# Kernel optimization log

Hardware: AMD Instinct MI355X
Metric: run time of the kernel (lower is better)

## Reference

```python
import jax, jax.numpy as jnp
import numpy as np

B, S, D, H = 2, 2048, 768, 12
DK = D // H


def setup_inputs() -> dict:
    key = jax.random.key(0)
    ks = jax.random.split(key, 12)
    s = 1.0 / np.sqrt(D)
    inp = {
        "query": jax.random.normal(ks[0], (B, S, D), jnp.float32),
        "key_": jax.random.normal(ks[1], (B, S, D), jnp.float32),
        "value": jax.random.normal(ks[2], (B, S, D), jnp.float32),
        # causal mask: 1 where attention allowed, 0 where blocked
        "mask": jnp.tril(jnp.ones((S, S), jnp.int32))[None, None, :, :],
        "W_q": jax.random.normal(ks[3], (D, D), jnp.float32) * s,
        "b_q": jnp.zeros((D,), jnp.float32),
        "W_k": jax.random.normal(ks[4], (D, D), jnp.float32) * s,
        "b_k": jnp.zeros((D,), jnp.float32),
        "W_v": jax.random.normal(ks[5], (D, D), jnp.float32) * s,
        "b_v": jnp.zeros((D,), jnp.float32),
        "W_o": jax.random.normal(ks[6], (D, D), jnp.float32) * s,
        "b_o": jnp.zeros((D,), jnp.float32),
    }
    return inp


def reference(query, key_, value, mask, W_q, b_q, W_k, b_k, W_v, b_v, W_o, b_o):
    # Linear projections (torch Linear: x @ W.T + b; here W stored as [in,out])
    Q = query @ W_q + b_q
    K = key_ @ W_k + b_k
    V = value @ W_v + b_v
    # [B,S,D] -> [B,H,S,dk]
    Q = Q.reshape(B, S, H, DK).transpose(0, 2, 1, 3)
    K = K.reshape(B, S, H, DK).transpose(0, 2, 1, 3)
    V = V.reshape(B, S, H, DK).transpose(0, 2, 1, 3)
    # NOTE: original module does NOT scale by 1/sqrt(d_k) -- faithful.
    scores = jnp.einsum('bhqd,bhkd->bhqk', Q, K)  # [B,H,S,S]
    scores = jnp.where(mask == 0, -jnp.inf, scores)
    attn = jax.nn.softmax(scores, axis=-1)
    out = jnp.einsum('bhqk,bhkd->bhqd', attn, V)  # [B,H,S,dk]
    out = out.transpose(0, 2, 1, 3).reshape(B, S, D)
    return out @ W_o + b_o
```

## Files before the change

### kernel.cpp

```cpp
#include <hip/hip_runtime.h>
#include <hip/hip_bf16.h>
#include <math.h>
#include <stdint.h>

constexpr int BATCH  = 2;
constexpr int SEQ    = 2048;
constexpr int DMODEL = 768;
constexpr int NH     = 12;
constexpr int HD     = 64;
constexpr int NTOK   = BATCH * SEQ;
constexpr float LOG2E = 1.4426950408889634f;

typedef __attribute__((ext_vector_type(8))) short     short8;
typedef __attribute__((ext_vector_type(8))) _Float16  half8;
typedef __attribute__((ext_vector_type(4))) float     floatx4;

#define DEVINL __device__ __forceinline__

DEVINL floatx4 mfma16(short8 a, short8 b, floatx4 c) {
    return __builtin_amdgcn_mfma_f32_16x16x32_bf16(a, b, c, 0, 0, 0);
}
DEVINL floatx4 mfma16h(half8 a, half8 b, floatx4 c) {
    return __builtin_amdgcn_mfma_f32_16x16x32_f16(a, b, c, 0, 0, 0);
}
DEVINL __hip_bfloat16 f2b(float x) { return __float2bfloat16(x); }

DEVINL void load16_lds(const void* g, void* l) {
    __builtin_amdgcn_global_load_lds(
        reinterpret_cast<const __attribute__((address_space(1))) unsigned int*>(
            reinterpret_cast<uintptr_t>(g)),
        reinterpret_cast<__attribute__((address_space(3))) unsigned int*>(
            reinterpret_cast<uintptr_t>(l)),
        16, 0, 0);
}

__global__ void pack_wt4(const float* __restrict__ W0, const float* __restrict__ W1,
                         const float* __restrict__ W2, const float* __restrict__ W3,
                         _Float16* H0, _Float16* H1, _Float16* H2, _Float16* H3) {
    int z = blockIdx.z;
    const float* W = (z == 0) ? W0 : (z == 1) ? W1 : (z == 2) ? W2 : W3;
    _Float16* H = (z == 0) ? H0 : (z == 1) ? H1 : (z == 2) ? H2 : H3;
    float sc = (z == 0) ? LOG2E : 1.0f;
    __shared__ float t[32][33];
    int k0 = blockIdx.x * 32, n0 = blockIdx.y * 32;
    int tx = threadIdx.x, ty = threadIdx.y;
    for (int i = ty; i < 32; i += 8)
        t[i][tx] = W[(size_t)(k0 + i) * DMODEL + n0 + tx];
    __syncthreads();
    for (int i = ty; i < 32; i += 8)
        H[(size_t)(n0 + i) * DMODEL + k0 + tx] = (_Float16)(t[tx][i] * sc);
}

__global__ void conv_h(const float* __restrict__ q, const float* __restrict__ k,
                       const float* __restrict__ v,
                       _Float16* qf, _Float16* kf, _Float16* vf) {
    int y = blockIdx.y;
    const float* src = (y == 0) ? q : (y == 1) ? k : v;
    _Float16* dst = (y == 0) ? qf : (y == 1) ? kf : vf;
    size_t base = ((size_t)blockIdx.x * 256 + threadIdx.x) * 8;
    float4 a = *(const float4*)(src + base);
    float4 b = *(const float4*)(src + base + 4);
    half8 o;
    o[0] = (_Float16)a.x; o[1] = (_Float16)a.y; o[2] = (_Float16)a.z; o[3] = (_Float16)a.w;
    o[4] = (_Float16)b.x; o[5] = (_Float16)b.y; o[6] = (_Float16)b.z; o[7] = (_Float16)b.w;
    *(half8*)(dst + base) = o;
}

DEVINL void stage_ab(const uint16_t* A, const uint16_t* B,
                     char* buf, int m0, int n0, int k0, int tid, int wv) {
#pragma unroll
    for (int i = 0; i < 4; ++i) {
        int e = i * 256 + tid;
        int row = e >> 3, c8 = (e & 7) ^ (row & 7);
        load16_lds(A + (size_t)(m0 + row) * DMODEL + k0 + c8 * 8,
                   buf + i * 4096 + wv * 1024);
    }
#pragma unroll
    for (int i = 0; i < 2; ++i) {
        int e = i * 256 + tid;
        int row = e >> 3, c8 = (e & 7) ^ (row & 7);
        load16_lds(B + (size_t)(n0 + row) * DMODEL + k0 + c8 * 8,
                   buf + 16384 + i * 4096 + wv * 1024);
    }
}

__global__ __launch_bounds__(256) void gemm_qkv(
    const uint16_t* __restrict__ qf, const uint16_t* __restrict__ kf,
    const uint16_t* __restrict__ vf,
    const uint16_t* __restrict__ Wq, const uint16_t* __restrict__ Wk,
    const uint16_t* __restrict__ Wv,
    const float* __restrict__ bq, const float* __restrict__ bk,
    const float* __restrict__ bv,
    _Float16* Qf, _Float16* Kf, __hip_bfloat16* Vt) {
    __shared__ __align__(16) char smem[49152];

    int z = blockIdx.z;
    const uint16_t* A = (z == 0) ? qf : (z == 1) ? kf : vf;
    const uint16_t* B = (z == 0) ? Wq : (z == 1) ? Wk : Wv;
    const float* bias = (z == 0) ? bq : (z == 1) ? bk : bv;
    float bscale = (z == 0) ? LOG2E : 1.0f;

    int tid = threadIdx.x;
    int wv = tid >> 6, lane = tid & 63, quad = lane >> 4, ln = lane & 15;
    int mw = wv & 1, nw = wv >> 1;
    int m0 = blockIdx.x * 128, n0 = blockIdx.y * 64;
    int sw = (ln & 7) * 16;

    floatx4 acc[4][2];
#pragma unroll
    for (int f = 0; f < 4; ++f)
#pragma unroll
        for (int g = 0; g < 2; ++g) acc[f][g] = floatx4{0.f, 0.f, 0.f, 0.f};

    stage_ab(A, B, smem, m0, n0, 0, tid, wv);

    for (int s = 0; s < 12; ++s) {
        __syncthreads();
        if (s + 1 < 12)
            stage_ab(A, B, smem + ((s + 1) & 1) * 24576, m0, n0, (s + 1) * 64, tid, wv);
        char* buf = smem + (s & 1) * 24576;
#pragma unroll
        for (int ks = 0; ks < 2; ++ks) {
            half8 ah[4], bh2[2];
#pragma unroll
            for (int f = 0; f < 4; ++f) {
                int row = mw * 64 + f * 16 + ln;
                ah[f] = *(const half8*)(buf + row * 128 + ((ks * 64 + quad * 16) ^ sw));
            }
#pragma unroll
            for (int g = 0; g < 2; ++g) {
                int row = nw * 32 + g * 16 + ln;
                bh2[g] = *(const half8*)(buf + 16384 + row * 128 + ((ks * 64 + quad * 16) ^ sw));
            }
#pragma unroll
            for (int f = 0; f < 4; ++f)
#pragma unroll
                for (int g = 0; g < 2; ++g)
                    acc[f][g] = mfma16h(ah[f], bh2[g], acc[f][g]);
        }
    }

    if (z == 2) {
        __syncthreads();
        __hip_bfloat16* T = (__hip_bfloat16*)smem;
#pragma unroll
        for (int f = 0; f < 4; ++f)
#pragma unroll
            for (int g = 0; g < 2; ++g) {
                int nl = nw * 32 + g * 16 + ln;
                float bvv = bias[n0 + nl];
#pragma unroll
                for (int rr = 0; rr < 4; ++rr) {
                    int ml = mw * 64 + f * 16 + quad * 4 + rr;
                    T[nl * 136 + ml] = f2b(acc[f][g][rr] + bvv);
                }
            }
        __syncthreads();
        int h = n0 >> 6, b = m0 >> 11;
        __hip_bfloat16* dst = Vt + (size_t)(b * NH + h) * HD * SEQ;
#pragma unroll
        for (int i = 0; i < 4; ++i) {
            int cid = i * 256 + tid;
            int d = cid >> 4, ch = cid & 15;
            short8 v = *(const short8*)(T + d * 136 + ch * 8);
            *(short8*)(dst + (size_t)d * SEQ + (m0 & (SEQ - 1)) + ch * 8) = v;
        }
    } else {
        _Float16* o0 = (z == 0) ? Qf : Kf;
#pragma unroll
        for (int f = 0; f < 4; ++f)
#pragma unroll
            for (int g = 0; g < 2; ++g) {
                int ncol = n0 + nw * 32 + g * 16 + ln;
                float bvv = bias[ncol] * bscale;
#pragma unroll
                for (int rr = 0; rr < 4; ++rr) {
                    int mrow = m0 + mw * 64 + f * 16 + quad * 4 + rr;
                    int b = mrow >> 11, s = mrow & (SEQ - 1);
                    int h = ncol >> 6, d = ncol & (HD - 1);
                    o0[((size_t)(b * NH + h) * SEQ + s) * HD + d] =
                        (_Float16)(acc[f][g][rr] + bvv);
                }
            }
    }
}

__global__ __launch_bounds__(256) void flash_k(
    const _Float16* __restrict__ Qf, const _Float16* __restrict__ Kf,
    const __hip_bfloat16* __restrict__ Vt,
    float* __restrict__ Oacc, float* __restrict__ Lacc) {
    int slot = blockIdx.x, bh = blockIdx.y;
    int qti, kv0, kv1;
    if (slot < 16) {
        qti = 15 - (slot >> 1);
        int hf = slot & 1;
        kv0 = hf * (qti + 1);
        kv1 = kv0 + qti + 1;
    } else {
        qti = 23 - slot;
        kv0 = 0;
        kv1 = 2 * qti + 2;
    }

    int tid = threadIdx.x;
    int wv = tid >> 6, lane = tid & 63, quad = lane >> 4, ln = lane & 15;
    int sw = (ln & 7) * 16;

    const _Float16* Qb = Qf + (size_t)bh * SEQ * HD;
    const uint16_t* Kb = (const uint16_t*)Kf + (size_t)bh * SEQ * HD;
    const uint16_t* Vb = (const uint16_t*)Vt + (size_t)bh * HD * SEQ;

    int qr0 = qti * 128 + wv * 32;

    __shared__ __align__(16) char smem[32768 + 4 * 16 * 72 * 2];
    __hip_bfloat16* sP = (__hip_bfloat16*)(smem + 32768) + wv * 16 * 72;

    auto stage = [&](int kv, int bsel) {
        char* buf = smem + bsel * 16384;
        int kb = kv * 64;
#pragma unroll
        for (int i = 0; i < 2; ++i) {
            int e = i * 256 + tid;
            int row = e >> 3, c8 = (e & 7) ^ (row & 7);
            int ldso = i * 4096 + wv * 1024;
            load16_lds(Kb + (size_t)(kb + row) * HD + c8 * 8, buf + ldso);
            load16_lds(Vb + (size_t)row * SEQ + kb + c8 * 8, buf + 8192 + ldso);
        }
    };

    stage(kv0, 0);

    half8 aQ[2][2];
#pragma unroll
    for (int rg = 0; rg < 2; ++rg)
#pragma unroll
        for (int ks = 0; ks < 2; ++ks)
            aQ[rg][ks] = *(const half8*)(Qb + (size_t)(qr0 + rg * 16 + ln) * HD +
                                         ks * 32 + quad * 8);

    short8 vone;
#pragma unroll
    for (int i = 0; i < 8; ++i) vone[i] = (short)0x3F80;

    floatx4 accO[2][4], accL[2];
#pragma unroll
    for (int rg = 0; rg < 2; ++rg) {
        accL[rg] = floatx4{0.f, 0.f, 0.f, 0.f};
#pragma unroll
        for (int j = 0; j < 4; ++j) accO[rg][j] = floatx4{0.f, 0.f, 0.f, 0.f};
    }

    for (int kv = kv0; kv < kv1; ++kv) {
        int ib = (kv - kv0) & 1;
        __syncthreads();
        if (kv + 1 < kv1) stage(kv + 1, ib ^ 1);
        const char* sK = smem + ib * 16384;
        const char* sV = sK + 8192;
        int kb = kv * 64;

        floatx4 accS[2][4];
#pragma unroll
        for (int rg = 0; rg < 2; ++rg)
#pragma unroll
            for (int cc = 0; cc < 4; ++cc) accS[rg][cc] = floatx4{0.f, 0.f, 0.f, 0.f};
#pragma unroll
        for (int cc = 0; cc < 4; ++cc)
#pragma unroll
            for (int ks = 0; ks < 2; ++ks) {
                int off = (cc * 16 + ln) * 128 + ((ks * 64 + quad * 16) ^ sw);
                half8 bK = *(const half8*)(sK + off);
                accS[0][cc] = mfma16h(aQ[0][ks], bK, accS[0][cc]);
                accS[1][cc] = mfma16h(aQ[1][ks], bK, accS[1][cc]);
            }

        short8 aP[2][2];
#pragma unroll
        for (int rg = 0; rg < 2; ++rg) {
            bool domask = (kb + 63 > qr0 + rg * 16);
#pragma unroll
            for (int rr = 0; rr < 4; ++rr) {
                int qg = qr0 + rg * 16 + quad * 4 + rr;
#pragma unroll
                for (int cc = 0; cc < 4; ++cc) {
                    float s = accS[rg][cc][rr];
                    if (domask && (kb + cc * 16 + ln > qg)) s = -INFINITY;
                    sP[(quad * 4 + rr) * 72 + cc * 16 + ln] =
                        f2b(__builtin_amdgcn_exp2f(s));
                }
            }
#pragma unroll
            for (int ks = 0; ks < 2; ++ks)
                aP[rg][ks] = *(const short8*)(sP + ln * 72 + ks * 32 + quad * 8);
            accL[rg] = mfma16(aP[rg][0], vone, accL[rg]);
            accL[rg] = mfma16(aP[rg][1], vone, accL[rg]);
        }

#pragma unroll
        for (int cc = 0; cc < 4; ++cc)
#pragma unroll
            for (int ks = 0; ks < 2; ++ks) {
                int off = (cc * 16 + ln) * 128 + ((ks * 64 + quad * 16) ^ sw);
                short8 bV = *(const short8*)(sV + off);
                accO[0][cc] = mfma16(aP[0][ks], bV, accO[0][cc]);
                accO[1][cc] = mfma16(aP[1][ks], bV, accO[1][cc]);
            }
    }

    float* Ob = Oacc + (size_t)bh * SEQ * HD;
#pragma unroll
    for (int rg = 0; rg < 2; ++rg)
#pragma unroll
        for (int cc = 0; cc < 4; ++cc)
#pragma unroll
            for (int rr = 0; rr < 4; ++rr) {
                int s = qr0 + rg * 16 + quad * 4 + rr;
                unsafeAtomicAdd(&Ob[(size_t)s * HD + cc * 16 + ln], accO[rg][cc][rr]);
            }
    if (ln == 0) {
#pragma unroll
        for (int rg = 0; rg < 2; ++rg)
#pragma unroll
            for (int rr = 0; rr < 4; ++rr)
                unsafeAtomicAdd(&Lacc[bh * SEQ + qr0 + rg * 16 + quad * 4 + rr],
                                accL[rg][rr]);
    }
}

__global__ void combine_k(const float* __restrict__ Oacc, const float* __restrict__ Lacc,
                          _Float16* __restrict__ attn) {
    int idx = blockIdx.x * 256 + threadIdx.x;
    int d8 = idx & 7;
    int rest = idx >> 3;
    int s = rest & (SEQ - 1);
    int bh = rest >> 11;
    int b = bh / NH, h = bh % NH;
    float inv = 1.0f / Lacc[bh * SEQ + s];
    const float* src = Oacc + ((size_t)bh * SEQ + s) * HD + d8 * 8;
    float4 a = *(const float4*)src;
    float4 c = *(const float4*)(src + 4);
    half8 o;
    o[0] = (_Float16)(a.x * inv); o[1] = (_Float16)(a.y * inv);
    o[2] = (_Float16)(a.z * inv); o[3] = (_Float16)(a.w * inv);
    o[4] = (_Float16)(c.x * inv); o[5] = (_Float16)(c.y * inv);
    o[6] = (_Float16)(c.z * inv); o[7] = (_Float16)(c.w * inv);
    *(half8*)(attn + ((size_t)(b * SEQ + s)) * DMODEL + h * HD + d8 * 8) = o;
}

__global__ __launch_bounds__(256) void gemm_o(
    const uint16_t* __restrict__ A, const uint16_t* __restrict__ B,
    const float* __restrict__ bias, float* __restrict__ out) {
    __shared__ __align__(16) char smem[49152];

    int tid = threadIdx.x;
    int wv = tid >> 6, lane = tid & 63, quad = lane >> 4, ln = lane & 15;
    int mw = wv & 1, nw = wv >> 1;
    int m0 = blockIdx.x * 128, n0 = blockIdx.y * 64;
    int sw = (ln & 7) * 16;

    floatx4 acc[4][2];
#pragma unroll
    for (int f = 0; f < 4; ++f)
#pragma unroll
        for (int g = 0; g < 2; ++g) acc[f][g] = floatx4{0.f, 0.f, 0.f, 0.f};

    stage_ab(A, B, smem, m0, n0, 0, tid, wv);

    for (int s = 0; s < 12; ++s) {
        __syncthreads();
        if (s + 1 < 12)
            stage_ab(A, B, smem + ((s + 1) & 1) * 24576, m0, n0, (s + 1) * 64, tid, wv);
        char* buf = smem + (s & 1) * 24576;
#pragma unroll
        for (int ks = 0; ks < 2; ++ks) {
            half8 ah[4], bh2[2];
#pragma unroll
            for (int f = 0; f < 4; ++f) {
                int row = mw * 64 + f * 16 + ln;
                ah[f] = *(const half8*)(buf + row * 128 + ((ks * 64 + quad * 16) ^ sw));
            }
#pragma unroll
            for (int g = 0; g < 2; ++g) {
                int row = nw * 32 + g * 16 + ln;
                bh2[g] = *(const half8*)(buf + 16384 + row * 128 + ((ks * 64 + quad * 16) ^ sw));
            }
#pragma unroll
            for (int f = 0; f < 4; ++f)
#pragma unroll
                for (int g = 0; g < 2; ++g)
                    acc[f][g] = mfma16h(ah[f], bh2[g], acc[f][g]);
        }
    }
#pragma unroll
    for (int f = 0; f < 4; ++f)
#pragma unroll
        for (int g = 0; g < 2; ++g) {
            int ncol = n0 + nw * 32 + g * 16 + ln;
            float bvv = bias[ncol];
#pragma unroll
            for (int rr = 0; rr < 4; ++rr) {
                int mrow = m0 + mw * 64 + f * 16 + quad * 4 + rr;
                out[(size_t)mrow * DMODEL + ncol] = acc[f][g][rr] + bvv;
            }
        }
}

extern "C" void kernel_launch(void* const* d_in, const int* in_sizes, int n_in,
                              void* d_out, int out_size, void* d_ws, size_t ws_size,
                              hipStream_t stream) {
    const float* query = (const float*)d_in[0];
    const float* key_  = (const float*)d_in[1];
    const float* value = (const float*)d_in[2];
    const float* W_q = (const float*)d_in[4];
    const float* b_q = (const float*)d_in[5];
    const float* W_k = (const float*)d_in[6];
    const float* b_k = (const float*)d_in[7];
    const float* W_v = (const float*)d_in[8];
    const float* b_v = (const float*)d_in[9];
    const float* W_o = (const float*)d_in[10];
    const float* b_o = (const float*)d_in[11];

    constexpr size_t WSZ = (size_t)DMODEL * DMODEL;
    constexpr size_t QSZ = (size_t)BATCH * NH * SEQ * HD;
    constexpr size_t OSZ = QSZ;
    constexpr size_t LSZ = (size_t)BATCH * NH * SEQ;

    char* w = (char*)d_ws;
    _Float16* Wq = (_Float16*)w; w += WSZ * 2;
    _Float16* Wk = (_Float16*)w; w += WSZ * 2;
    _Float16* Wv = (_Float16*)w; w += WSZ * 2;
    _Float16* Wo = (_Float16*)w; w += WSZ * 2;
    _Float16* qf = (_Float16*)w; w += QSZ * 2;
    _Float16* kf = (_Float16*)w; w += QSZ * 2;
    _Float16* vf = (_Float16*)w; w += QSZ * 2;
    _Float16* Qf_ = (_Float16*)w; w += QSZ * 2;
    _Float16* Kf_ = (_Float16*)w; w += QSZ * 2;
    __hip_bfloat16* Vt_ = (__hip_bfloat16*)w; w += QSZ * 2;
    _Float16* attn_ = (_Float16*)w; w += QSZ * 2;
    float* Oacc = (float*)qf;
    float* Lacc = Oacc + OSZ;

    pack_wt4<<<dim3(24, 24, 4), dim3(32, 8), 0, stream>>>(
        W_q, W_k, W_v, W_o, Wq, Wk, Wv, Wo);
    conv_h<<<dim3(NTOK * DMODEL / 2048, 3), 256, 0, stream>>>(
        query, key_, value, qf, kf, vf);

    gemm_qkv<<<dim3(NTOK / 128, DMODEL / 64, 3), 256, 0, stream>>>(
        (const uint16_t*)qf, (const uint16_t*)kf, (const uint16_t*)vf,
        (const uint16_t*)Wq, (const uint16_t*)Wk, (const uint16_t*)Wv,
        b_q, b_k, b_v, Qf_, Kf_, Vt_);

    (void)hipMemsetAsync(Oacc, 0, (OSZ + LSZ) * sizeof(float), stream);

    flash_k<<<dim3(24, BATCH * NH), 256, 0, stream>>>(Qf_, Kf_, Vt_, Oacc, Lacc);

    combine_k<<<dim3(BATCH * NH * SEQ * 8 / 256), 256, 0, stream>>>(Oacc, Lacc, attn_);

    gemm_o<<<dim3(NTOK / 128, DMODEL / 64), 256, 0, stream>>>(
        (const uint16_t*)attn_, (const uint16_t*)Wo, b_o, (float*)d_out);
}
```

Measured before the change: 198.7 us.

## Merge prep kernels and stage GEMM epilogues through LDS for coalesced stores

Folds the weight transpose/pack and the input fp16 conversion into a single launch using a z-dimension split with a grid-stride loop. It also rewrites the Q/K projection epilogue and the output-projection epilogue to write results into swizzled shared memory first, then issue 16-byte coalesced global stores instead of scattered 2- or 4-byte per-lane stores. This removes one kernel launch and uncoalesced write traffic, at the cost of extra barriers and LDS round trips.

```diff
diff --git a/kernel.cpp b/kernel.cpp
--- a/kernel.cpp
+++ b/kernel.cpp
@@ -34,36 +34,43 @@
         16, 0, 0);
 }
 
-__global__ void pack_wt4(const float* __restrict__ W0, const float* __restrict__ W1,
-                         const float* __restrict__ W2, const float* __restrict__ W3,
-                         _Float16* H0, _Float16* H1, _Float16* H2, _Float16* H3) {
-    int z = blockIdx.z;
-    const float* W = (z == 0) ? W0 : (z == 1) ? W1 : (z == 2) ? W2 : W3;
-    _Float16* H = (z == 0) ? H0 : (z == 1) ? H1 : (z == 2) ? H2 : H3;
-    float sc = (z == 0) ? LOG2E : 1.0f;
-    __shared__ float t[32][33];
-    int k0 = blockIdx.x * 32, n0 = blockIdx.y * 32;
-    int tx = threadIdx.x, ty = threadIdx.y;
-    for (int i = ty; i < 32; i += 8)
-        t[i][tx] = W[(size_t)(k0 + i) * DMODEL + n0 + tx];
-    __syncthreads();
-    for (int i = ty; i < 32; i += 8)
-        H[(size_t)(n0 + i) * DMODEL + k0 + tx] = (_Float16)(t[tx][i] * sc);
-}
-
-__global__ void conv_h(const float* __restrict__ q, const float* __restrict__ k,
+__global__ void prep_k(const float* __restrict__ W0, const float* __restrict__ W1,
+                       const float* __restrict__ W2, const float* __restrict__ W3,
+                       _Float16* H0, _Float16* H1, _Float16* H2, _Float16* H3,
+                       const float* __restrict__ q, const float* __restrict__ k,
                        const float* __restrict__ v,
                        _Float16* qf, _Float16* kf, _Float16* vf) {
-    int y = blockIdx.y;
-    const float* src = (y == 0) ? q : (y == 1) ? k : v;
-    _Float16* dst = (y == 0) ? qf : (y == 1) ? kf : vf;
-    size_t base = ((size_t)blockIdx.x * 256 + threadIdx.x) * 8;
-    float4 a = *(const float4*)(src + base);
-    float4 b = *(const float4*)(src + base + 4);
-    half8 o;
-    o[0] = (_Float16)a.x; o[1] = (_Float16)a.y; o[2] = (_Float16)a.z; o[3] = (_Float16)a.w;
-    o[4] = (_Float16)b.x; o[5] = (_Float16)b.y; o[6] = (_Float16)b.z; o[7] = (_Float16)b.w;
-    *(half8*)(dst + base) = o;
+    int z = blockIdx.z;
+    int tid = threadIdx.x;
+    if (z < 4) {
+        const float* W = (z == 0) ? W0 : (z == 1) ? W1 : (z == 2) ? W2 : W3;
+        _Float16* H = (z == 0) ? H0 : (z == 1) ? H1 : (z == 2) ? H2 : H3;
+        float sc = (z == 0) ? LOG2E : 1.0f;
+        __shared__ float t[32][33];
+        int k0 = blockIdx.x * 32, n0 = blockIdx.y * 32;
+        int tx = tid & 31, ty = tid >> 5;
+        for (int i = ty; i < 32; i += 8)
+            t[i][tx] = W[(size_t)(k0 + i) * DMODEL + n0 + tx];
+        __syncthreads();
+        for (int i = ty; i < 32; i += 8)
+            H[(size_t)(n0 + i) * DMODEL + k0 + tx] = (_Float16)(t[tx][i] * sc);
+    } else {
+        const float* src = (z == 4) ? q : (z == 5) ? k : v;
+        _Float16* dst = (z == 4) ? qf : (z == 5) ? kf : vf;
+        constexpr int NCH = NTOK * DMODEL / 8;
+        int flat = (blockIdx.y * 24 + blockIdx.x) * 256 + tid;
+        for (int c = flat; c < NCH; c += 24 * 24 * 256) {
+            size_t base = (size_t)c * 8;
+            float4 a = *(const float4*)(src + base);
+            float4 b = *(const float4*)(src + base + 4);
+            half8 o;
+            o[0] = (_Float16)a.x; o[1] = (_Float16)a.y;
+            o[2] = (_Float16)a.z; o[3] = (_Float16)a.w;
+            o[4] = (_Float16)b.x; o[5] = (_Float16)b.y;
+            o[6] = (_Float16)b.z; o[7] = (_Float16)b.w;
+            *(half8*)(dst + base) = o;
+        }
+    }
 }
 
 DEVINL void stage_ab(const uint16_t* A, const uint16_t* B,
@@ -139,9 +146,10 @@
                     acc[f][g] = mfma16h(ah[f], bh2[g], acc[f][g]);
         }
     }
-
+    __syncthreads();
+
+    int b = m0 >> 11, s0 = m0 & (SEQ - 1), h = n0 >> 6;
     if (z == 2) {
-        __syncthreads();
         __hip_bfloat16* T = (__hip_bfloat16*)smem;
 #pragma unroll
         for (int f = 0; f < 4; ++f)
@@ -156,32 +164,40 @@
                 }
             }
         __syncthreads();
-        int h = n0 >> 6, b = m0 >> 11;
         __hip_bfloat16* dst = Vt + (size_t)(b * NH + h) * HD * SEQ;
 #pragma unroll
         for (int i = 0; i < 4; ++i) {
             int cid = i * 256 + tid;
             int d = cid >> 4, ch = cid & 15;
             short8 v = *(const short8*)(T + d * 136 + ch * 8);
-            *(short8*)(dst + (size_t)d * SEQ + (m0 & (SEQ - 1)) + ch * 8) = v;
+            *(short8*)(dst + (size_t)d * SEQ + s0 + ch * 8) = v;
         }
     } else {
         _Float16* o0 = (z == 0) ? Qf : Kf;
+        uint16_t* T = (uint16_t*)smem;
 #pragma unroll
         for (int f = 0; f < 4; ++f)
 #pragma unroll
             for (int g = 0; g < 2; ++g) {
-                int ncol = n0 + nw * 32 + g * 16 + ln;
-                float bvv = bias[ncol] * bscale;
+                int nl = nw * 32 + g * 16 + ln;
+                float bvv = bias[n0 + nl] * bscale;
 #pragma unroll
                 for (int rr = 0; rr < 4; ++rr) {
-                    int mrow = m0 + mw * 64 + f * 16 + quad * 4 + rr;
-                    int b = mrow >> 11, s = mrow & (SEQ - 1);
-                    int h = ncol >> 6, d = ncol & (HD - 1);
-                    o0[((size_t)(b * NH + h) * SEQ + s) * HD + d] =
-                        (_Float16)(acc[f][g][rr] + bvv);
+                    int ml = mw * 64 + f * 16 + quad * 4 + rr;
+                    int phys = (((nl >> 3) ^ (ml & 7)) << 3) | (nl & 7);
+                    _Float16 hv = (_Float16)(acc[f][g][rr] + bvv);
+                    T[ml * 64 + phys] = *(uint16_t*)&hv;
                 }
             }
+        __syncthreads();
+        _Float16* dst = o0 + ((size_t)(b * NH + h) * SEQ + s0) * HD;
+#pragma unroll
+        for (int i = 0; i < 4; ++i) {
+            int cid = i * 256 + tid;
+            int row = cid >> 3, j = cid & 7;
+            short8 v = *(const short8*)(T + row * 64 + ((j ^ (row & 7)) << 3));
+            *(short8*)(dst + (size_t)row * HD + j * 8) = v;
+        }
     }
 }
 
@@ -390,18 +406,29 @@
                     acc[f][g] = mfma16h(ah[f], bh2[g], acc[f][g]);
         }
     }
+    __syncthreads();
+    float* T = (float*)smem;
 #pragma unroll
     for (int f = 0; f < 4; ++f)
 #pragma unroll
         for (int g = 0; g < 2; ++g) {
-            int ncol = n0 + nw * 32 + g * 16 + ln;
-            float bvv = bias[ncol];
+            int nl = nw * 32 + g * 16 + ln;
+            float bvv = bias[n0 + nl];
 #pragma unroll
             for (int rr = 0; rr < 4; ++rr) {
-                int mrow = m0 + mw * 64 + f * 16 + quad * 4 + rr;
-                out[(size_t)mrow * DMODEL + ncol] = acc[f][g][rr] + bvv;
-            }
-        }
+                int ml = mw * 64 + f * 16 + quad * 4 + rr;
+                int phys = (((nl >> 2) ^ (ml & 15)) << 2) | (nl & 3);
+                T[ml * 64 + phys] = acc[f][g][rr] + bvv;
+            }
+        }
+    __syncthreads();
+#pragma unroll
+    for (int i = 0; i < 8; ++i) {
+        int cid = i * 256 + tid;
+        int row = cid >> 4, j = cid & 15;
+        float4 v = *(const float4*)(T + row * 64 + ((j ^ (row & 15)) << 2));
+        *(float4*)(out + (size_t)(m0 + row) * DMODEL + n0 + j * 4) = v;
+    }
 }
 
 extern "C" void kernel_launch(void* const* d_in, const int* in_sizes, int n_in,
@@ -439,10 +466,8 @@
     float* Oacc = (float*)qf;
     float* Lacc = Oacc + OSZ;
 
-    pack_wt4<<<dim3(24, 24, 4), dim3(32, 8), 0, stream>>>(
-        W_q, W_k, W_v, W_o, Wq, Wk, Wv, Wo);
-    conv_h<<<dim3(NTOK * DMODEL / 2048, 3), 256, 0, stream>>>(
-        query, key_, value, qf, kf, vf);
+    prep_k<<<dim3(24, 24, 7), 256, 0, stream>>>(
+        W_q, W_k, W_v, W_o, Wq, Wk, Wv, Wo, query, key_, value, qf, kf, vf);
 
     gemm_qkv<<<dim3(NTOK / 128, DMODEL / 64, 3), 256, 0, stream>>>(
         (const uint16_t*)qf, (const uint16_t*)kf, (const uint16_t*)vf,
```

New measurement: 200.3 us. No clear change (+0.8%).
